# Kernel optimization log

Hardware: AMD Instinct MI355X
Metric: run time of the kernel (lower is better)

## Reference

```python
import jax, jax.numpy as jnp
import numpy as np

B = 1024      # batch
M = 4096      # num_meas
W = 2         # width_per_meas
L = 2         # num_hidden_layers
Z = 64        # num_vae_latent
H = M * W     # hidden_dim = 8192


def setup_inputs() -> dict:
    key = jax.random.key(0)
    ks = jax.random.split(key, 24)

    def nrm(i, shape, scale=0.02):
        return (jax.random.normal(ks[i], shape, dtype=jnp.float32) * scale)

    return {
        "x": jax.random.normal(ks[0], (B, M), dtype=jnp.float32),
        "eps": jax.random.normal(ks[1], (B, Z), dtype=jnp.float32),
        # encoder (dense)
        "enc1_w": nrm(2, (M, M)), "enc1_b": nrm(3, (M,)),
        "enc2_w": nrm(4, (M, M)), "enc2_b": nrm(5, (M,)),
        "mu_w": nrm(6, (Z, M)), "mu_b": nrm(7, (Z,)),
        "lv_w": nrm(8, (Z, M)), "lv_b": nrm(9, (Z,)),
        # decoder mean branch: fulcon dense, hidden/output in block form
        "mean_ful_w": nrm(10, (H, Z)), "mean_ful_b": nrm(11, (H,)),
        "mean_h_w": nrm(12, (L, M, W, W)), "mean_h_b": nrm(13, (L, H)),
        "mean_out_w": nrm(14, (M, W)), "mean_out_b": nrm(15, (M,)),
        # decoder logcov branch
        "cov_ful_w": nrm(16, (H, Z)), "cov_ful_b": nrm(17, (H,)),
        "cov_h_w": nrm(18, (L, M, W, W)), "cov_h_b": nrm(19, (L, H)),
        "cov_out_w": nrm(20, (M, W)), "cov_out_b": nrm(21, (M,)),
    }


def _decoder_branch(z, ful_w, ful_b, h_w, h_b, out_w, out_b):
    # fulcon: dense latent -> hidden, then sigmoid
    a = jax.nn.sigmoid(z @ ful_w.T + ful_b)            # [B, H]
    a = a.reshape(B, M, W)                             # block-diag structure
    for l in range(L):
        # grouped block-diagonal matmul == masked dense linear of the original
        a = jax.nn.sigmoid(
            jnp.einsum('bmw,mvw->bmv', a, h_w[l]) + h_b[l].reshape(M, W)
        )
    # output mask blocks are [1, W] per measurement
    return jnp.einsum('bmw,mw->bm', a, out_w) + out_b  # [B, M]


def reference(x, eps, enc1_w, enc1_b, enc2_w, enc2_b, mu_w, mu_b, lv_w, lv_b,
              mean_ful_w, mean_ful_b, mean_h_w, mean_h_b, mean_out_w, mean_out_b,
              cov_ful_w, cov_ful_b, cov_h_w, cov_h_b, cov_out_w, cov_out_b):
    # encoder
    h = jax.nn.relu(x @ enc1_w.T + enc1_b)
    h = jax.nn.relu(h @ enc2_w.T + enc2_b)
    mu = h @ mu_w.T + mu_b
    logvar = h @ lv_w.T + lv_b
    # reparameterization (training mode, eps supplied)
    z = mu + jnp.exp(0.5 * logvar) * eps
    # decoder
    x_recon = _decoder_branch(z, mean_ful_w, mean_ful_b, mean_h_w, mean_h_b,
                              mean_out_w, mean_out_b)
    logcov = _decoder_branch(z, cov_ful_w, cov_ful_b, cov_h_w, cov_h_b,
                             cov_out_w, cov_out_b)
    return (x_recon, logcov, mu, logvar)
```

## Files before the change

kernel.cpp:

```cpp
#include <hip/hip_runtime.h>
#include <hip/hip_bf16.h>
#include <stdint.h>

typedef __hip_bfloat16 bf16;
typedef __bf16 bf16x8 __attribute__((ext_vector_type(8)));
typedef float f32x4 __attribute__((ext_vector_type(4)));

#define NB 1024
#define NM 4096
#define NZ 64
#define NH 8192

__device__ __forceinline__ float bf2f(bf16 x) { return __bfloat162float(x); }
__device__ __forceinline__ bf16 f2bf(float x) { return __float2bfloat16(x); }
__device__ __forceinline__ float sigf(float x) { return 1.f / (1.f + __expf(-x)); }

__global__ __launch_bounds__(256) void cvt_f32_bf16(const float* __restrict__ src,
                                                    bf16* __restrict__ dst, int n4) {
  const int i = blockIdx.x * 256 + threadIdx.x;
  if (i >= n4) return;
  const float4 v = ((const float4*)src)[i];
  bf16 o[4] = {f2bf(v.x), f2bf(v.y), f2bf(v.z), f2bf(v.w)};
  *(short4*)&dst[i * 4] = *(short4*)o;
}

__global__ void zero_f32(float* p, int n) {
  int i = blockIdx.x * blockDim.x + threadIdx.x;
  if (i < n) p[i] = 0.f;
}

#define VMW8 asm volatile("s_waitcnt vmcnt(8)" ::: "memory")
#define VMW0 asm volatile("s_waitcnt vmcnt(0)" ::: "memory")
#define LGKM0 asm volatile("s_waitcnt lgkmcnt(0)" ::: "memory")

__global__ __launch_bounds__(256) void gemm_nt(const bf16* __restrict__ A,
                                               const float* __restrict__ W,
                                               const float* __restrict__ bias,
                                               bf16* __restrict__ C,
                                               int K, int N) {
  __shared__ __attribute__((aligned(16))) bf16 smA[3][128 * 64];
  __shared__ __attribute__((aligned(16))) bf16 smB[2][64 * 64];
  const int tid  = threadIdx.x;
  const int lane = tid & 63;
  const int w    = tid >> 6;
  const int wr   = w >> 1;
  const int wc   = w & 1;

  const int lid  = blockIdx.y * 8 + blockIdx.x;
  const int wgid = (lid & 7) * 64 + (lid >> 3);
  const int row0 = (wgid & 7) * 128;
  const int col0 = (wgid >> 3) * 64;

  f32x4 acc[4][2];
#pragma unroll
  for (int i = 0; i < 4; i++)
#pragma unroll
    for (int j = 0; j < 2; j++) acc[i][j] = (f32x4){0.f, 0.f, 0.f, 0.f};

  const int swr = tid >> 2;
  const int swk = (tid & 3) * 16;
  const float* wp = W + (size_t)(col0 + swr) * K + swk;
  const int swz = (swr & 7) << 3;
  const int woff0 = swr * 64 + ((swk + 0) ^ swz);
  const int woff1 = swr * 64 + ((swk + 8) ^ swz);

  auto load_W = [&](float4 (&wv)[4], int kk) {
    wv[0] = *(const float4*)(wp + kk);
    wv[1] = *(const float4*)(wp + kk + 4);
    wv[2] = *(const float4*)(wp + kk + 8);
    wv[3] = *(const float4*)(wp + kk + 12);
  };

  auto stage_A = [&](int slot, int kk) {
#pragma unroll
    for (int q = 0; q < 4; q++) {
      const int chunk = q * 256 + w * 64 + lane;
      const int r  = chunk >> 3;
      const int ke = ((chunk & 7) ^ (r & 7)) * 8;
      __builtin_amdgcn_global_load_lds(
          (__attribute__((address_space(1))) unsigned int*)(A + (size_t)(row0 + r) * K + (kk + ke)),
          (__attribute__((address_space(3))) unsigned int*)(&smA[slot][(q * 256 + w * 64) * 8]),
          16, 0, 0);
    }
  };

  auto write_W = [&](int slot, const float4 (&wv)[4]) {
    bf16 t[16] = {f2bf(wv[0].x), f2bf(wv[0].y), f2bf(wv[0].z), f2bf(wv[0].w),
                  f2bf(wv[1].x), f2bf(wv[1].y), f2bf(wv[1].z), f2bf(wv[1].w),
                  f2bf(wv[2].x), f2bf(wv[2].y), f2bf(wv[2].z), f2bf(wv[2].w),
                  f2bf(wv[3].x), f2bf(wv[3].y), f2bf(wv[3].z), f2bf(wv[3].w)};
    *(bf16x8*)&smB[slot][woff0] = ((bf16x8*)t)[0];
    *(bf16x8*)&smB[slot][woff1] = ((bf16x8*)t)[1];
  };

  auto compute = [&](int sa, int ws) {
#pragma unroll
    for (int ks = 0; ks < 64; ks += 32) {
      const int kq = ks + (lane >> 4) * 8;
      bf16x8 af[4], bfr[2];
#pragma unroll
      for (int i = 0; i < 4; i++) {
        const int r = wr * 64 + i * 16 + (lane & 15);
        af[i] = *(const bf16x8*)&smA[sa][r * 64 + (kq ^ ((r & 7) << 3))];
      }
#pragma unroll
      for (int j = 0; j < 2; j++) {
        const int r = wc * 32 + j * 16 + (lane & 15);
        bfr[j] = *(const bf16x8*)&smB[ws][r * 64 + (kq ^ ((r & 7) << 3))];
      }
#pragma unroll
      for (int i = 0; i < 4; i++)
#pragma unroll
        for (int j = 0; j < 2; j++)
          acc[i][j] = __builtin_amdgcn_mfma_f32_16x16x32_bf16(af[i], bfr[j], acc[i][j], 0, 0, 0);
    }
  };

  const int K64 = K >> 6;
  float4 wA[4], wB[4];

  load_W(wA, 0);
  stage_A(0, 0);
  asm volatile("" ::: "memory");
  load_W(wB, 64);
  stage_A(1, 64);

  int sa = 0;
  for (int i = 0; i + 2 < K64; i += 2) {
    const int nx  = (sa + 1 == 3) ? 0 : sa + 1;
    const int nnx = (nx + 1 == 3) ? 0 : nx + 1;
    VMW8;
    write_W(0, wA);
    LGKM0;
    __builtin_amdgcn_s_barrier();
    __builtin_amdgcn_sched_barrier(0);
    load_W(wA, (i + 2) * 64);
    stage_A(nnx, (i + 2) * 64);
    compute(sa, 0);
    VMW8;
    write_W(1, wB);
    LGKM0;
    __builtin_amdgcn_s_barrier();
    __builtin_amdgcn_sched_barrier(0);
    load_W(wB, (i + 3) * 64);
    stage_A(sa, (i + 3) * 64);
    compute(nx, 1);
    sa = nnx;
  }
  VMW8;
  write_W(0, wA);
  LGKM0;
  __builtin_amdgcn_s_barrier();
  __builtin_amdgcn_sched_barrier(0);
  compute(sa, 0);
  VMW0;
  write_W(1, wB);
  LGKM0;
  __builtin_amdgcn_s_barrier();
  __builtin_amdgcn_sched_barrier(0);
  compute((sa + 1 == 3) ? 0 : sa + 1, 1);

#pragma unroll
  for (int i = 0; i < 4; i++) {
#pragma unroll
    for (int j = 0; j < 2; j++) {
      const int cc = col0 + wc * 32 + j * 16 + (lane & 15);
      const float bs = bias[cc];
#pragma unroll
      for (int t = 0; t < 4; t++) {
        const int rr = row0 + wr * 64 + i * 16 + (lane >> 4) * 4 + t;
        float v = acc[i][j][t] + bs;
        v = v > 0.f ? v : 0.f;
        C[(size_t)rr * N + cc] = f2bf(v);
      }
    }
  }
}

__global__ __launch_bounds__(256) void mulv_splitk(const bf16* __restrict__ h2,
                                                   const float* __restrict__ muw,
                                                   const float* __restrict__ lvw,
                                                   float* __restrict__ zpre) {
  __shared__ float sA[32][33];
  __shared__ float sW[32][128];
  const int tid = threadIdx.x;
  const int b0 = blockIdx.x * 32;
  const int k0 = blockIdx.y * 256;
  const int tj = tid & 15;
  const int tb = tid >> 4;
  float acc[2][8];
#pragma unroll
  for (int i = 0; i < 2; i++)
#pragma unroll
    for (int j = 0; j < 8; j++) acc[i][j] = 0.f;

  const int lb = tid >> 3, lk = (tid & 7) * 4;
  const int wj = tid >> 1, wk = (tid & 1) * 16;
  const float* wrow = (wj < 64) ? (muw + (size_t)wj * NM) : (lvw + (size_t)(wj - 64) * NM);

  for (int kc = 0; kc < 256; kc += 32) {
    __syncthreads();
    {
      const uint2 v = *(const uint2*)(h2 + (size_t)(b0 + lb) * NM + (k0 + kc + lk));
      sA[lk + 0][lb] = __uint_as_float(v.x << 16);
      sA[lk + 1][lb] = __uint_as_float(v.x & 0xffff0000u);
      sA[lk + 2][lb] = __uint_as_float(v.y << 16);
      sA[lk + 3][lb] = __uint_as_float(v.y & 0xffff0000u);
      const float* q = wrow + (k0 + kc + wk);
#pragma unroll
      for (int i = 0; i < 4; i++) {
        const float4 f = *(const float4*)(q + i * 4);
        sW[wk + i * 4 + 0][wj] = f.x;
        sW[wk + i * 4 + 1][wj] = f.y;
        sW[wk + i * 4 + 2][wj] = f.z;
        sW[wk + i * 4 + 3][wj] = f.w;
      }
    }
    __syncthreads();
#pragma unroll
    for (int k = 0; k < 32; k++) {
      const float av0 = sA[k][tb * 2 + 0];
      const float av1 = sA[k][tb * 2 + 1];
      float wv[8];
#pragma unroll
      for (int j = 0; j < 8; j++) wv[j] = sW[k][16 * j + tj];
#pragma unroll
      for (int j = 0; j < 8; j++) {
        acc[0][j] += av0 * wv[j];
        acc[1][j] += av1 * wv[j];
      }
    }
  }
#pragma unroll
  for (int i = 0; i < 2; i++)
#pragma unroll
    for (int j = 0; j < 8; j++)
      atomicAdd(&zpre[(size_t)(b0 + tb * 2 + i) * 128 + 16 * j + tj], acc[i][j]);
}

__global__ void zfin(const float* __restrict__ zpre, const float* __restrict__ eps,
                     const float* __restrict__ mub, const float* __restrict__ lvb,
                     float* __restrict__ out_mu, float* __restrict__ out_lv,
                     float* __restrict__ z) {
  const int i = blockIdx.x * 256 + threadIdx.x;
  const int b = i >> 6, j = i & 63;
  const float mu = zpre[(size_t)b * 128 + j] + mub[j];
  const float lv = zpre[(size_t)b * 128 + 64 + j] + lvb[j];
  const float zz = mu + expf(0.5f * lv) * eps[i];
  out_mu[i] = mu;
  out_lv[i] = lv;
  z[i] = zz;
}

__global__ __launch_bounds__(256) void dec_fused(
    const float* __restrict__ z,
    const float* __restrict__ fw, const float* __restrict__ fb,
    const float* __restrict__ hw, const float* __restrict__ hb,
    const float* __restrict__ ow, const float* __restrict__ ob,
    float* __restrict__ out) {
  __shared__ __attribute__((aligned(16))) float sZ[64][68];
  __shared__ __attribute__((aligned(16))) float sFW[64][132];
  const int tid = threadIdx.x;
  const int b0 = blockIdx.x * 64;
  const int m0 = blockIdx.y * 256;
  const int mi = blockIdx.z;
  {
    const int r  = tid >> 2;
    const int c0 = (tid & 3) * 16;
    const float* p = z + (size_t)(b0 + r) * NZ + c0;
#pragma unroll
    for (int i = 0; i < 16; i++) sZ[c0 + i][r] = p[i];
  }

  const int bq = tid >> 5;
  const int tm = tid & 31;
  const int mb = m0 + mi * 64;

  {
    const int R0 = 2 * mb;
#pragma unroll
    for (int q = 0; q < 8; q++) {
      const int v = tid + q * 256;
      const int grow = v >> 4;
      const int gk = (v & 15) * 4;
      const float4 f4 = *(const float4*)&fw[(size_t)(R0 + grow) * NZ + gk];
      sFW[gk + 0][grow] = f4.x;
      sFW[gk + 1][grow] = f4.y;
      sFW[gk + 2][grow] = f4.z;
      sFW[gk + 3][grow] = f4.w;
    }
  }
  __syncthreads();

  const int mA = mb + 2 * tm;
  const float4 fb4 = *(const float4*)&fb[2 * mA];
  float aA0[8], aA1[8], aB0[8], aB1[8];
#pragma unroll
  for (int j = 0; j < 8; j++) { aA0[j] = fb4.x; aA1[j] = fb4.y; aB0[j] = fb4.z; aB1[j] = fb4.w; }

#pragma unroll 8
  for (int k = 0; k < 64; k++) {
    const float4 w4 = *(const float4*)&sFW[k][4 * tm];
    const float4 z0 = *(const float4*)&sZ[k][bq * 8 + 0];
    const float4 z1 = *(const float4*)&sZ[k][bq * 8 + 4];
    const float zv[8] = {z0.x, z0.y, z0.z, z0.w, z1.x, z1.y, z1.z, z1.w};
#pragma unroll
    for (int j = 0; j < 8; j++) {
      aA0[j] += zv[j] * w4.x;
      aA1[j] += zv[j] * w4.y;
      aB0[j] += zv[j] * w4.z;
      aB1[j] += zv[j] * w4.w;
    }
  }

  float4 hwA[2], hwB[2], hb4[2];
#pragma unroll
  for (int l = 0; l < 2; l++) {
    hwA[l] = *(const float4*)&hw[((size_t)l * NM + mA) * 4];
    hwB[l] = *(const float4*)&hw[((size_t)l * NM + mA) * 4 + 4];
    hb4[l] = *(const float4*)&hb[(size_t)l * NH + 2 * mA];
  }
  const float4 o4 = *(const float4*)&ow[2 * mA];
  const float2 ob2 = *(const float2*)&ob[mA];
#pragma unroll
  for (int j = 0; j < 8; j++) {
    float a0 = sigf(aA0[j]), a1 = sigf(aA1[j]);
    float b0v = sigf(aB0[j]), b1v = sigf(aB1[j]);
#pragma unroll
    for (int l = 0; l < 2; l++) {
      const float nA0 = sigf(hwA[l].x * a0 + hwA[l].y * a1 + hb4[l].x);
      const float nA1 = sigf(hwA[l].z * a0 + hwA[l].w * a1 + hb4[l].y);
      const float nB0 = sigf(hwB[l].x * b0v + hwB[l].y * b1v + hb4[l].z);
      const float nB1 = sigf(hwB[l].z * b0v + hwB[l].w * b1v + hb4[l].w);
      a0 = nA0; a1 = nA1; b0v = nB0; b1v = nB1;
    }
    const float outA = a0 * o4.x + a1 * o4.y + ob2.x;
    const float outB = b0v * o4.z + b1v * o4.w + ob2.y;
    float2 o2; o2.x = outA; o2.y = outB;
    *(float2*)&out[(size_t)(b0 + bq * 8 + j) * NM + mA] = o2;
  }
}

extern "C" void kernel_launch(void* const* d_in, const int* in_sizes, int n_in,
                              void* d_out, int out_size, void* d_ws, size_t ws_size,
                              hipStream_t stream) {
  const float* x   = (const float*)d_in[0];
  const float* eps = (const float*)d_in[1];
  const float* e1w = (const float*)d_in[2];
  const float* e1b = (const float*)d_in[3];
  const float* e2w = (const float*)d_in[4];
  const float* e2b = (const float*)d_in[5];
  const float* muw = (const float*)d_in[6];
  const float* mub = (const float*)d_in[7];
  const float* lvw = (const float*)d_in[8];
  const float* lvb = (const float*)d_in[9];
  const float* mfw = (const float*)d_in[10];
  const float* mfb = (const float*)d_in[11];
  const float* mhw = (const float*)d_in[12];
  const float* mhb = (const float*)d_in[13];
  const float* mow = (const float*)d_in[14];
  const float* mob = (const float*)d_in[15];
  const float* cfw = (const float*)d_in[16];
  const float* cfb = (const float*)d_in[17];
  const float* chw = (const float*)d_in[18];
  const float* chb = (const float*)d_in[19];
  const float* cow = (const float*)d_in[20];
  const float* cob = (const float*)d_in[21];

  char* ob_ = (char*)d_out;
  float* out_x  = (float*)ob_;
  float* out_lc = (float*)(ob_ + (16u << 20));
  float* out_mu = out_x + (size_t)2 * NB * NM;
  float* out_lv = out_mu + (size_t)NB * NZ;
  bf16* h1 = (bf16*)ob_;
  bf16* xb = (bf16*)(ob_ + (16u << 20));
  bf16* h2 = xb;

  float* zpre = (float*)d_ws;
  float* z    = (float*)((char*)d_ws + (1u << 19));

  cvt_f32_bf16<<<dim3(4096), 256, 0, stream>>>(x, xb, NB * NM / 4);
  zero_f32<<<dim3(512), 256, 0, stream>>>(zpre, NB * 128);
  gemm_nt<<<dim3(8, 64), 256, 0, stream>>>(xb, e1w, e1b, h1, NM, NM);
  gemm_nt<<<dim3(8, 64), 256, 0, stream>>>(h1, e2w, e2b, h2, NM, NM);
  mulv_splitk<<<dim3(32, 16), 256, 0, stream>>>(h2, muw, lvw, zpre);
  zfin<<<dim3(256), 256, 0, stream>>>(zpre, eps, mub, lvb, out_mu, out_lv, z);
  dec_fused<<<dim3(16, 16, 4), 256, 0, stream>>>(z, mfw, mfb, mhw, mhb, mow, mob, out_x);
  dec_fused<<<dim3(16, 16, 4), 256, 0, stream>>>(z, cfw, cfb, chw, chb, cow, cob, out_lc);
}
```

Measured before the change: 440.1 us.

## Use 512-thread workgroups in encoder GEMM and halve decoder weight LDS staging

```diff
diff --git a/kernel.cpp b/kernel.cpp
--- a/kernel.cpp
+++ b/kernel.cpp
@@ -29,11 +29,11 @@
   if (i < n) p[i] = 0.f;
 }
 
-#define VMW8 asm volatile("s_waitcnt vmcnt(8)" ::: "memory")
+#define VMW4 asm volatile("s_waitcnt vmcnt(4)" ::: "memory")
 #define VMW0 asm volatile("s_waitcnt vmcnt(0)" ::: "memory")
 #define LGKM0 asm volatile("s_waitcnt lgkmcnt(0)" ::: "memory")
 
-__global__ __launch_bounds__(256) void gemm_nt(const bf16* __restrict__ A,
+__global__ __launch_bounds__(512) void gemm_nt(const bf16* __restrict__ A,
                                                const float* __restrict__ W,
                                                const float* __restrict__ bias,
                                                bf16* __restrict__ C,
@@ -51,56 +51,49 @@
   const int row0 = (wgid & 7) * 128;
   const int col0 = (wgid >> 3) * 64;
 
-  f32x4 acc[4][2];
-#pragma unroll
-  for (int i = 0; i < 4; i++)
+  f32x4 acc[2][2];
+#pragma unroll
+  for (int i = 0; i < 2; i++)
 #pragma unroll
     for (int j = 0; j < 2; j++) acc[i][j] = (f32x4){0.f, 0.f, 0.f, 0.f};
 
-  const int swr = tid >> 2;
-  const int swk = (tid & 3) * 16;
+  const int swr = tid >> 3;
+  const int swk = (tid & 7) * 8;
   const float* wp = W + (size_t)(col0 + swr) * K + swk;
-  const int swz = (swr & 7) << 3;
-  const int woff0 = swr * 64 + ((swk + 0) ^ swz);
-  const int woff1 = swr * 64 + ((swk + 8) ^ swz);
-
-  auto load_W = [&](float4 (&wv)[4], int kk) {
+  const int woff = swr * 64 + (swk ^ ((swr & 7) << 3));
+
+  auto load_W = [&](float4 (&wv)[2], int kk) {
     wv[0] = *(const float4*)(wp + kk);
     wv[1] = *(const float4*)(wp + kk + 4);
-    wv[2] = *(const float4*)(wp + kk + 8);
-    wv[3] = *(const float4*)(wp + kk + 12);
   };
 
   auto stage_A = [&](int slot, int kk) {
 #pragma unroll
-    for (int q = 0; q < 4; q++) {
-      const int chunk = q * 256 + w * 64 + lane;
+    for (int q = 0; q < 2; q++) {
+      const int chunk = q * 512 + w * 64 + lane;
       const int r  = chunk >> 3;
       const int ke = ((chunk & 7) ^ (r & 7)) * 8;
       __builtin_amdgcn_global_load_lds(
           (__attribute__((address_space(1))) unsigned int*)(A + (size_t)(row0 + r) * K + (kk + ke)),
-          (__attribute__((address_space(3))) unsigned int*)(&smA[slot][(q * 256 + w * 64) * 8]),
+          (__attribute__((address_space(3))) unsigned int*)(&smA[slot][(q * 512 + w * 64) * 8]),
           16, 0, 0);
     }
   };
 
-  auto write_W = [&](int slot, const float4 (&wv)[4]) {
-    bf16 t[16] = {f2bf(wv[0].x), f2bf(wv[0].y), f2bf(wv[0].z), f2bf(wv[0].w),
-                  f2bf(wv[1].x), f2bf(wv[1].y), f2bf(wv[1].z), f2bf(wv[1].w),
-                  f2bf(wv[2].x), f2bf(wv[2].y), f2bf(wv[2].z), f2bf(wv[2].w),
-                  f2bf(wv[3].x), f2bf(wv[3].y), f2bf(wv[3].z), f2bf(wv[3].w)};
-    *(bf16x8*)&smB[slot][woff0] = ((bf16x8*)t)[0];
-    *(bf16x8*)&smB[slot][woff1] = ((bf16x8*)t)[1];
+  auto write_W = [&](int slot, const float4 (&wv)[2]) {
+    bf16 t[8] = {f2bf(wv[0].x), f2bf(wv[0].y), f2bf(wv[0].z), f2bf(wv[0].w),
+                 f2bf(wv[1].x), f2bf(wv[1].y), f2bf(wv[1].z), f2bf(wv[1].w)};
+    *(bf16x8*)&smB[slot][woff] = *(bf16x8*)t;
   };
 
   auto compute = [&](int sa, int ws) {
 #pragma unroll
     for (int ks = 0; ks < 64; ks += 32) {
       const int kq = ks + (lane >> 4) * 8;
-      bf16x8 af[4], bfr[2];
-#pragma unroll
-      for (int i = 0; i < 4; i++) {
-        const int r = wr * 64 + i * 16 + (lane & 15);
+      bf16x8 af[2], bfr[2];
+#pragma unroll
+      for (int i = 0; i < 2; i++) {
+        const int r = wr * 32 + i * 16 + (lane & 15);
         af[i] = *(const bf16x8*)&smA[sa][r * 64 + (kq ^ ((r & 7) << 3))];
       }
 #pragma unroll
@@ -109,7 +102,7 @@
         bfr[j] = *(const bf16x8*)&smB[ws][r * 64 + (kq ^ ((r & 7) << 3))];
       }
 #pragma unroll
-      for (int i = 0; i < 4; i++)
+      for (int i = 0; i < 2; i++)
 #pragma unroll
         for (int j = 0; j < 2; j++)
           acc[i][j] = __builtin_amdgcn_mfma_f32_16x16x32_bf16(af[i], bfr[j], acc[i][j], 0, 0, 0);
@@ -117,7 +110,7 @@
   };
 
   const int K64 = K >> 6;
-  float4 wA[4], wB[4];
+  float4 wA[2], wB[2];
 
   load_W(wA, 0);
   stage_A(0, 0);
@@ -129,7 +122,7 @@
   for (int i = 0; i + 2 < K64; i += 2) {
     const int nx  = (sa + 1 == 3) ? 0 : sa + 1;
     const int nnx = (nx + 1 == 3) ? 0 : nx + 1;
-    VMW8;
+    VMW4;
     write_W(0, wA);
     LGKM0;
     __builtin_amdgcn_s_barrier();
@@ -137,7 +130,7 @@
     load_W(wA, (i + 2) * 64);
     stage_A(nnx, (i + 2) * 64);
     compute(sa, 0);
-    VMW8;
+    VMW4;
     write_W(1, wB);
     LGKM0;
     __builtin_amdgcn_s_barrier();
@@ -147,7 +140,7 @@
     compute(nx, 1);
     sa = nnx;
   }
-  VMW8;
+  VMW4;
   write_W(0, wA);
   LGKM0;
   __builtin_amdgcn_s_barrier();
@@ -161,14 +154,14 @@
   compute((sa + 1 == 3) ? 0 : sa + 1, 1);
 
 #pragma unroll
-  for (int i = 0; i < 4; i++) {
+  for (int i = 0; i < 2; i++) {
 #pragma unroll
     for (int j = 0; j < 2; j++) {
       const int cc = col0 + wc * 32 + j * 16 + (lane & 15);
       const float bs = bias[cc];
 #pragma unroll
       for (int t = 0; t < 4; t++) {
-        const int rr = row0 + wr * 64 + i * 16 + (lane >> 4) * 4 + t;
+        const int rr = row0 + wr * 32 + i * 16 + (lane >> 4) * 4 + t;
         float v = acc[i][j][t] + bs;
         v = v > 0.f ? v : 0.f;
         C[(size_t)rr * N + cc] = f2bf(v);
@@ -259,7 +252,7 @@
     const float* __restrict__ ow, const float* __restrict__ ob,
     float* __restrict__ out) {
   __shared__ __attribute__((aligned(16))) float sZ[64][68];
-  __shared__ __attribute__((aligned(16))) float sFW[64][132];
+  __shared__ __attribute__((aligned(16))) float sFW[32][132];
   const int tid = threadIdx.x;
   const int b0 = blockIdx.x * 64;
   const int m0 = blockIdx.y * 256;
@@ -275,41 +268,46 @@
   const int bq = tid >> 5;
   const int tm = tid & 31;
   const int mb = m0 + mi * 64;
-
-  {
-    const int R0 = 2 * mb;
-#pragma unroll
-    for (int q = 0; q < 8; q++) {
-      const int v = tid + q * 256;
-      const int grow = v >> 4;
-      const int gk = (v & 15) * 4;
-      const float4 f4 = *(const float4*)&fw[(size_t)(R0 + grow) * NZ + gk];
-      sFW[gk + 0][grow] = f4.x;
-      sFW[gk + 1][grow] = f4.y;
-      sFW[gk + 2][grow] = f4.z;
-      sFW[gk + 3][grow] = f4.w;
-    }
-  }
-  __syncthreads();
-
   const int mA = mb + 2 * tm;
+
   const float4 fb4 = *(const float4*)&fb[2 * mA];
   float aA0[8], aA1[8], aB0[8], aB1[8];
 #pragma unroll
   for (int j = 0; j < 8; j++) { aA0[j] = fb4.x; aA1[j] = fb4.y; aB0[j] = fb4.z; aB1[j] = fb4.w; }
 
+  const int R0 = 2 * mb;
+#pragma unroll
+  for (int kh = 0; kh < 2; kh++) {
+    __syncthreads();
+    {
+#pragma unroll
+      for (int q = 0; q < 4; q++) {
+        const int v = tid + q * 256;
+        const int grow = v >> 3;
+        const int gk = (v & 7) * 4;
+        const float4 f4 = *(const float4*)&fw[(size_t)(R0 + grow) * NZ + kh * 32 + gk];
+        sFW[gk + 0][grow] = f4.x;
+        sFW[gk + 1][grow] = f4.y;
+        sFW[gk + 2][grow] = f4.z;
+        sFW[gk + 3][grow] = f4.w;
+      }
+    }
+    __syncthreads();
+
 #pragma unroll 8
-  for (int k = 0; k < 64; k++) {
-    const float4 w4 = *(const float4*)&sFW[k][4 * tm];
-    const float4 z0 = *(const float4*)&sZ[k][bq * 8 + 0];
-    const float4 z1 = *(const float4*)&sZ[k][bq * 8 + 4];
-    const float zv[8] = {z0.x, z0.y, z0.z, z0.w, z1.x, z1.y, z1.z, z1.w};
-#pragma unroll
-    for (int j = 0; j < 8; j++) {
-      aA0[j] += zv[j] * w4.x;
-      aA1[j] += zv[j] * w4.y;
-      aB0[j] += zv[j] * w4.z;
-      aB1[j] += zv[j] * w4.w;
+    for (int k2 = 0; k2 < 32; k2++) {
+      const int k = kh * 32 + k2;
+      const float4 w4 = *(const float4*)&sFW[k2][4 * tm];
+      const float4 z0 = *(const float4*)&sZ[k][bq * 8 + 0];
+      const float4 z1 = *(const float4*)&sZ[k][bq * 8 + 4];
+      const float zv[8] = {z0.x, z0.y, z0.z, z0.w, z1.x, z1.y, z1.z, z1.w};
+#pragma unroll
+      for (int j = 0; j < 8; j++) {
+        aA0[j] += zv[j] * w4.x;
+        aA1[j] += zv[j] * w4.y;
+        aB0[j] += zv[j] * w4.z;
+        aB1[j] += zv[j] * w4.w;
+      }
     }
   }
 
@@ -381,8 +379,8 @@
 
   cvt_f32_bf16<<<dim3(4096), 256, 0, stream>>>(x, xb, NB * NM / 4);
   zero_f32<<<dim3(512), 256, 0, stream>>>(zpre, NB * 128);
-  gemm_nt<<<dim3(8, 64), 256, 0, stream>>>(xb, e1w, e1b, h1, NM, NM);
-  gemm_nt<<<dim3(8, 64), 256, 0, stream>>>(h1, e2w, e2b, h2, NM, NM);
+  gemm_nt<<<dim3(8, 64), 512, 0, stream>>>(xb, e1w, e1b, h1, NM, NM);
+  gemm_nt<<<dim3(8, 64), 512, 0, stream>>>(h1, e2w, e2b, h2, NM, NM);
   mulv_splitk<<<dim3(32, 16), 256, 0, stream>>>(h2, muw, lvw, zpre);
   zfin<<<dim3(256), 256, 0, stream>>>(zpre, eps, mub, lvb, out_mu, out_lv, z);
   dec_fused<<<dim3(16, 16, 4), 256, 0, stream>>>(z, mfw, mfb, mhw, mhb, mow, mob, out_x);
```

New measurement: 426.4 us. -3.1%, faster.
